# Kernel tuning notes

Measured on AMD Instinct MI355X. Metric: run time of the kernel, lower is better.

Reference implementation:

```python
import jax, jax.numpy as jnp
import numpy as np

E = 256      # embed_dim
H = 4        # num_heads
EXP = 4      # expansion_factor
B, C, R = 8, 32, 255  # batch, max_cols, rows (seq = R+1 with CLS)
LN_EPS = 1e-5


def setup_inputs() -> dict:
    key = jax.random.key(0)
    ks = jax.random.split(key, 16)
    s = 0.02
    return {
        "x": jax.random.normal(ks[0], (B, C, R, E), jnp.float32),
        "real_cols": jax.random.randint(ks[1], (B,), 0, C + 1),
        "real_rows": jax.random.randint(ks[2], (B,), 0, R + 1),
        "cls_token": jax.random.normal(ks[3], (E,), jnp.float32) * s,
        # MHA in_proj (torch packs q,k,v as (3E, E)) and out_proj
        "w_qkv": jax.random.normal(ks[4], (3 * E, E), jnp.float32) * s,
        "b_qkv": jnp.zeros((3 * E,), jnp.float32),
        "w_out": jax.random.normal(ks[5], (E, E), jnp.float32) * s,
        "b_out": jnp.zeros((E,), jnp.float32),
        # LayerNorm
        "ln_g": jnp.ones((E,), jnp.float32),
        "ln_b": jnp.zeros((E,), jnp.float32),
        # FFN: Linear(E, 4E) -> ReLU -> Linear(4E, E)
        "w1": jax.random.normal(ks[6], (EXP * E, E), jnp.float32) * s,
        "b1": jnp.zeros((EXP * E,), jnp.float32),
        "w2": jax.random.normal(ks[7], (E, EXP * E), jnp.float32) * s,
        "b2": jnp.zeros((E,), jnp.float32),
    }


def reference(x, real_cols, real_rows, cls_token, w_qkv, b_qkv, w_out, b_out,
              ln_g, ln_b, w1, b1, w2, b2):
    Bn, Cn, Rn, En = x.shape
    S = Rn + 1
    Dh = En // H
    dt = x.dtype

    # prepend CLS token to every column's row sequence -> (B, C, S, E)
    cls = jnp.broadcast_to(cls_token.astype(dt), (Bn, Cn, 1, En))
    xc = jnp.concatenate([cls, x], axis=2)

    # fused qkv projection
    qkv = jnp.einsum('bcse,fe->bcsf', xc, w_qkv.astype(dt)) + b_qkv.astype(dt)
    q, k, v = jnp.split(qkv, 3, axis=-1)
    q = q.reshape(Bn, Cn, S, H, Dh)
    k = k.reshape(Bn, Cn, S, H, Dh)
    v = v.reshape(Bn, Cn, S, H, Dh)

    scale = 1.0 / np.sqrt(Dh).astype(np.float32)
    scores = jnp.einsum('bcqhd,bckhd->bchqk', q, k) * scale  # (B,C,H,S,S)

    # key_padding_mask: position 0 (CLS) always valid; row p (1..R) valid iff p <= nrow
    pos = jnp.arange(S)
    valid = (pos[None, :] == 0) | (pos[None, :] <= real_rows[:, None])  # (B, S)
    neg = jnp.asarray(-1e9, scores.dtype)
    scores = jnp.where(valid[:, None, None, None, :], scores, neg)

    attn = jax.nn.softmax(scores, axis=-1)
    ctx = jnp.einsum('bchqk,bckhd->bcqhd', attn, v).reshape(Bn, Cn, S, En)
    mha = jnp.einsum('bcse,fe->bcsf', ctx, w_out.astype(dt)) + b_out.astype(dt)

    # LayerNorm over E
    mu = mha.mean(axis=-1, keepdims=True)
    var = ((mha - mu) ** 2).mean(axis=-1, keepdims=True)
    ln = (mha - mu) * jax.lax.rsqrt(var + LN_EPS) * ln_g.astype(dt) + ln_b.astype(dt)

    # FFN with residual from ln (out = ln + ffn(ln))
    h = jax.nn.relu(jnp.einsum('bcse,fe->bcsf', ln, w1.astype(dt)) + b1.astype(dt))
    ffn = jnp.einsum('bcsf,ef->bcse', h, w2.astype(dt)) + b2.astype(dt)
    out = ln + ffn

    # rep_mode == 'cls': take CLS position; zero out padded columns
    rep = out[:, :, 0, :]  # (B, C, E)
    col_valid = (jnp.arange(Cn)[None, :] < real_cols[:, None]).astype(dt)
    return rep * col_valid[..., None]
```

## Files before the change

kernel.cpp:

```cpp
#include <hip/hip_runtime.h>
#include <hip/hip_bf16.h>
#include <math.h>

static constexpr int kC = 32, kR = 255, kE = 256;

__device__ float g_q0kv[768];
__device__ float g_qw[4 * 256];
__device__ float g_s0[4];
__device__ float g_qb[4];
__device__ float g_m[256 * 4 * 4];
__device__ float g_l[256 * 4 * 4];
__device__ float g_part[256 * 4 * 4 * 256];
__device__ unsigned short g_wv_bf[256 * 256];
__device__ unsigned short g_wout_bf[256 * 256];
__device__ unsigned short g_w1_bf[1024 * 256];
__device__ unsigned short g_w2_bf[256 * 1024];

__device__ inline unsigned short f2bf(float f) {
  __hip_bfloat16 h = __float2bfloat16(f);
  return __builtin_bit_cast(unsigned short, h);
}
__device__ inline float bflo(unsigned int u) { return __uint_as_float(u << 16); }
__device__ inline float bfhi(unsigned int u) { return __uint_as_float(u & 0xffff0000u); }

__global__ __launch_bounds__(256) void k_heads(const float* __restrict__ cls,
                                               const float* __restrict__ w_qkv,
                                               const float* __restrict__ b_qkv) {
  const int t = threadIdx.x, wvi = t >> 6, l = t & 63;
  const int h = blockIdx.x;
  __shared__ float q0h[64];
  __shared__ float kch[64];
  {
    const int r = t >> 1, half = t & 1;
    const int row = (r < 64) ? (h * 64 + r) : (256 + h * 64 + (r - 64));
    const float4* wp = (const float4*)(w_qkv + (size_t)row * 256 + half * 128);
    const float4* cp = (const float4*)cls + half * 32;
    float a = 0.f;
#pragma unroll 8
    for (int j = 0; j < 32; ++j) {
      float4 w4 = wp[j];
      float4 cv = cp[j];
      a += w4.x * cv.x + w4.y * cv.y + w4.z * cv.z + w4.w * cv.w;
    }
    a += __shfl_xor(a, 1);
    if (half == 0) {
      const float val = a + b_qkv[row];
      if (r < 64) q0h[r] = val; else kch[r - 64] = val;
    }
  }
  __syncthreads();

  float acc = 0.f;
#pragma unroll 8
  for (int j = 0; j < 64; ++j)
    acc += q0h[j] * w_qkv[(size_t)(256 + h * 64 + j) * 256 + t];
  g_qw[h * 256 + t] = acc * 0.125f;
  if (wvi == 0) {
    const float q = q0h[l];
    float pk = q * kch[l];
    float pb = q * b_qkv[256 + h * 64 + l];
#pragma unroll
    for (int m = 1; m < 64; m <<= 1) {
      pk += __shfl_xor(pk, m);
      pb += __shfl_xor(pb, m);
    }
    if (l == 0) {
      g_s0[h] = pk * 0.125f;
      g_qb[h] = pb * 0.125f;
    }
  }
}

__global__ __launch_bounds__(256) void k_attn(const float* __restrict__ x,
                                              const int* __restrict__ real_cols,
                                              const int* __restrict__ real_rows,
                                              const float* __restrict__ cls,
                                              const float* __restrict__ w_qkv,
                                              const float* __restrict__ b_qkv,
                                              const float* __restrict__ w_out,
                                              const float* __restrict__ w1,
                                              const float* __restrict__ w2) {
  const int t = threadIdx.x, wv = t >> 6, l = t & 63;
  const int bid = blockIdx.x;
  __shared__ __align__(16) char smem[71680];

  if (bid >= 1064) {
    const int row = 512 + (bid - 1064) * 4 + wv;
    float4 w4 = *((const float4*)(w_qkv + (size_t)row * 256) + l);
    float4 c4 = *((const float4*)cls + l);
    float a = w4.x * c4.x + w4.y * c4.y + w4.z * c4.z + w4.w * c4.w;
#pragma unroll
    for (int m = 1; m < 64; m <<= 1) a += __shfl_xor(a, m);
    if (l == 0) g_q0kv[row] = a + b_qkv[row];
    return;
  }

  if (bid >= 1024) {
    const int u = bid - 1024;
    const float* src;
    unsigned short* dst;
    int R, C, o0, e0;
    if (u < 4) { src = w_qkv + 512 * 256; dst = g_wv_bf; R = 256; C = 256; o0 = u * 64; e0 = 0; }
    else if (u < 8) { src = w_out; dst = g_wout_bf; R = 256; C = 256; o0 = (u - 4) * 64; e0 = 0; }
    else if (u < 24) { src = w1; dst = g_w1_bf; R = 1024; C = 256; o0 = (u - 8) * 64; e0 = 0; }
    else { const int v = u - 24; src = w2; dst = g_w2_bf; R = 256; C = 1024; o0 = (v >> 2) * 64; e0 = (v & 3) * 256; }

    unsigned short* tile = (unsigned short*)smem;
    for (int r = wv; r < 64; r += 4) {
      float4 v = *((const float4*)(src + (size_t)(o0 + r) * C + e0) + l);
      ushort4 ov;
      ov.x = f2bf(v.x); ov.y = f2bf(v.y); ov.z = f2bf(v.z); ov.w = f2bf(v.w);
      *(ushort4*)&tile[r * 260 + 4 * l] = ov;
    }
    __syncthreads();
    const int e80 = e0 >> 3;
    for (int e8l = wv; e8l < 32; e8l += 4) {
      const unsigned int* tp = (const unsigned int*)&tile[l * 260 + e8l * 8];
      uint4 o;
      o.x = tp[0]; o.y = tp[1]; o.z = tp[2]; o.w = tp[3];
      *(uint4*)(dst + ((size_t)(e80 + e8l) * R + o0 + l) * 8) = o;
    }
    return;
  }

  const int bc = bid >> 2, chunk = bid & 3;
  const int b = bc >> 5, c = bc & 31;
  if (c >= real_cols[b]) return;
  const int rr = real_rows[b];
  const int r0 = chunk * 64;
  const int nr = min(64, rr - r0);
  if (nr <= 0) return;

  float (*xs)[260] = (float(*)[260])smem;
  float (*qws)[256] = (float(*)[256])(smem + 66560);
  float (*ps)[64] = (float(*)[64])(smem + 70656);

#pragma unroll
  for (int i = 0; i < 4; ++i) qws[i][t] = g_qw[i * 256 + t];

  const float* xb = x + ((size_t)bc * kR + r0) * kE;
  for (int r = wv; r < nr; r += 4)
    *(float4*)&xs[r][4 * l] = *(const float4*)(xb + (size_t)r * kE + 4 * l);
  __syncthreads();

  const int h = wv, row = l;
  float acc = 0.f;
  const float4* qrow = (const float4*)&qws[h][0];
  const float4* xrow = (const float4*)&xs[row][0];
#pragma unroll 8
  for (int e4 = 0; e4 < 64; ++e4) {
    float4 q4 = qrow[e4];
    float4 x4 = xrow[e4];
    acc += q4.x * x4.x + q4.y * x4.y + q4.z * x4.z + q4.w * x4.w;
  }
  float s = (row < nr) ? acc + g_qb[h] : -1e30f;
  float mx = s;
#pragma unroll
  for (int m = 1; m < 64; m <<= 1) mx = fmaxf(mx, __shfl_xor(mx, m));
  float p = (row < nr) ? __expf(s - mx) : 0.f;
  float lsum = p;
#pragma unroll
  for (int m = 1; m < 64; m <<= 1) lsum += __shfl_xor(lsum, m);
  ps[h][row] = p;
  if (l == 0) {
    g_m[(bc * 4 + chunk) * 4 + h] = mx;
    g_l[(bc * 4 + chunk) * 4 + h] = lsum;
  }
  __syncthreads();

  float a0 = 0.f, a1 = 0.f, a2 = 0.f, a3 = 0.f;
  for (int r2 = 0; r2 < nr; ++r2) {
    float xv = xs[r2][t];
    a0 += ps[0][r2] * xv;
    a1 += ps[1][r2] * xv;
    a2 += ps[2][r2] * xv;
    a3 += ps[3][r2] * xv;
  }
  float* pp = g_part + (size_t)(bc * 4 + chunk) * 4 * 256;
  pp[0 * 256 + t] = a0;
  pp[1 * 256 + t] = a1;
  pp[2 * 256 + t] = a2;
  pp[3 * 256 + t] = a3;
}

__global__ __launch_bounds__(1024) void k_token(const int* __restrict__ real_cols,
                                                const int* __restrict__ real_rows,
                                                const float* __restrict__ b_qkv,
                                                const float* __restrict__ b_out,
                                                const float* __restrict__ ln_g,
                                                const float* __restrict__ ln_b,
                                                const float* __restrict__ b1,
                                                const float* __restrict__ b2,
                                                float* __restrict__ out) {
  const int bc = blockIdx.x, b = bc >> 5, c = bc & 31;
  const int t = threadIdx.x, wv = t >> 6, l = t & 63;
  if (c >= real_cols[b]) {
    if (t < 256) out[(size_t)bc * 256 + t] = 0.f;
    return;
  }
  const int rr = real_rows[b];
  const int nch = (rr + 63) >> 6;

  __shared__ float xb[4][256];
  __shared__ float part[4][256];
  __shared__ float ctxs[256];
  __shared__ float lns[256];
  __shared__ float hs[1024];
  __shared__ float al[4][4];
  __shared__ float p0s[4];
  __shared__ float rb[2][4];

  if (t < 4) {
    const int h = t;
    const float s0 = g_s0[h];
    float M = s0;
    for (int ch = 0; ch < nch; ++ch) M = fmaxf(M, g_m[(bc * 4 + ch) * 4 + h]);
    float lt = __expf(s0 - M);
    const float w0 = lt;
    float av[4] = {0.f, 0.f, 0.f, 0.f};
    for (int ch = 0; ch < nch; ++ch) {
      float e = __expf(g_m[(bc * 4 + ch) * 4 + h] - M);
      av[ch] = e;
      lt += g_l[(bc * 4 + ch) * 4 + h] * e;
    }
    const float inv = 1.f / lt;
#pragma unroll
    for (int ch = 0; ch < 4; ++ch) al[h][ch] = av[ch] * inv;
    p0s[h] = w0 * inv;
  }
  __syncthreads();

  {
    const int h = t >> 8, e = t & 255;
    float a = 0.f;
    for (int ch = 0; ch < nch; ++ch)
      a += al[h][ch] * g_part[(size_t)(bc * 4 + ch) * 4 * 256 + h * 256 + e];
    xb[h][e] = a;
  }
  __syncthreads();

  {
    const int f = t & 255, q = t >> 8, h = f >> 6;
    const uint4* wr = (const uint4*)g_wv_bf;
    const float4* v4p = (const float4*)&xb[h][0];
    float acc = 0.f;
#pragma unroll
    for (int i = 0; i < 8; ++i) {
      const int e8 = q * 8 + i;
      uint4 w = wr[e8 * 256 + f];
      float4 a = v4p[2 * e8], bb = v4p[2 * e8 + 1];
      acc += bflo(w.x) * a.x + bfhi(w.x) * a.y + bflo(w.y) * a.z + bfhi(w.y) * a.w +
             bflo(w.z) * bb.x + bfhi(w.z) * bb.y + bflo(w.w) * bb.z + bfhi(w.w) * bb.w;
    }
    part[q][f] = acc;
  }
  __syncthreads();
  if (t < 256) {
    const int h = t >> 6;
    const float p0 = p0s[h];
    ctxs[t] = part[0][t] + part[1][t] + part[2][t] + part[3][t] +
              p0 * g_q0kv[512 + t] + (1.f - p0) * b_qkv[512 + t];
  }
  __syncthreads();

  {
    const int g = t & 255, q = t >> 8;
    const uint4* wr = (const uint4*)g_wout_bf;
    const float4* c4 = (const float4*)&ctxs[0];
    float acc = 0.f;
#pragma unroll
    for (int i = 0; i < 8; ++i) {
      const int e8 = q * 8 + i;
      uint4 w = wr[e8 * 256 + g];
      float4 a = c4[2 * e8], bb = c4[2 * e8 + 1];
      acc += bflo(w.x) * a.x + bfhi(w.x) * a.y + bflo(w.y) * a.z + bfhi(w.y) * a.w +
             bflo(w.z) * bb.x + bfhi(w.z) * bb.y + bflo(w.w) * bb.z + bfhi(w.w) * bb.w;
    }
    part[q][g] = acc;
  }
  __syncthreads();
  float mh = 0.f;
  if (t < 256) {
    mh = part[0][t] + part[1][t] + part[2][t] + part[3][t] + b_out[t];
    float s1 = mh, s2 = mh * mh;
#pragma unroll
    for (int m = 1; m < 64; m <<= 1) {
      s1 += __shfl_xor(s1, m);
      s2 += __shfl_xor(s2, m);
    }
    if (l == 0) {
      rb[0][wv] = s1;
      rb[1][wv] = s2;
    }
  }
  __syncthreads();
  if (t < 256) {
    const float mu = (rb[0][0] + rb[0][1] + rb[0][2] + rb[0][3]) * (1.f / 256.f);
    const float msq = (rb[1][0] + rb[1][1] + rb[1][2] + rb[1][3]) * (1.f / 256.f);
    const float var = msq - mu * mu;
    lns[t] = (mh - mu) * rsqrtf(var + 1e-5f) * ln_g[t] + ln_b[t];
  }
  __syncthreads();

  {
    const uint4* wr = (const uint4*)g_w1_bf;
    float acc = b1[t];
#pragma unroll
    for (int e8 = 0; e8 < 32; ++e8) {
      uint4 w = wr[e8 * 1024 + t];
      const float4 a = *(const float4*)&lns[8 * e8];
      const float4 bbv = *(const float4*)&lns[8 * e8 + 4];
      acc += bflo(w.x) * a.x + bfhi(w.x) * a.y + bflo(w.y) * a.z + bfhi(w.y) * a.w +
             bflo(w.z) * bbv.x + bfhi(w.z) * bbv.y + bflo(w.w) * bbv.z + bfhi(w.w) * bbv.w;
    }
    hs[t] = fmaxf(acc, 0.f);
  }
  __syncthreads();

  {
    const int e = t & 255, q = t >> 8;
    const uint4* wr = (const uint4*)g_w2_bf;
    const float4* h4 = (const float4*)&hs[0];
    float acc = 0.f;
#pragma unroll 8
    for (int i = 0; i < 32; ++i) {
      const int f8 = q * 32 + i;
      uint4 w = wr[f8 * 256 + e];
      float4 a = h4[2 * f8], bb = h4[2 * f8 + 1];
      acc += bflo(w.x) * a.x + bfhi(w.x) * a.y + bflo(w.y) * a.z + bfhi(w.y) * a.w +
             bflo(w.z) * bb.x + bfhi(w.z) * bb.y + bflo(w.w) * bb.z + bfhi(w.w) * bb.w;
    }
    part[q][e] = acc;
  }
  __syncthreads();
  if (t < 256)
    out[(size_t)bc * 256 + t] =
        lns[t] + part[0][t] + part[1][t] + part[2][t] + part[3][t] + b2[t];
}

extern "C" void kernel_launch(void* const* d_in, const int* in_sizes, int n_in,
                              void* d_out, int out_size, void* d_ws, size_t ws_size,
                              hipStream_t stream) {
  const float* x = (const float*)d_in[0];
  const int* real_cols = (const int*)d_in[1];
  const int* real_rows = (const int*)d_in[2];
  const float* cls = (const float*)d_in[3];
  const float* w_qkv = (const float*)d_in[4];
  const float* b_qkv = (const float*)d_in[5];
  const float* w_out = (const float*)d_in[6];
  const float* b_out = (const float*)d_in[7];
  const float* ln_g = (const float*)d_in[8];
  const float* ln_b = (const float*)d_in[9];
  const float* w1 = (const float*)d_in[10];
  const float* b1 = (const float*)d_in[11];
  const float* w2 = (const float*)d_in[12];
  const float* b2 = (const float*)d_in[13];
  float* out = (float*)d_out;
  (void)in_sizes; (void)n_in; (void)out_size; (void)d_ws; (void)ws_size;

  k_heads<<<4, 256, 0, stream>>>(cls, w_qkv, b_qkv);
  k_attn<<<1128, 256, 0, stream>>>(x, real_cols, real_rows, cls, w_qkv, b_qkv, w_out, w1, w2);
  k_token<<<256, 1024, 0, stream>>>(real_cols, real_rows, b_qkv, b_out, ln_g, ln_b, b1, b2, out);
}
```

Before: 154.7 us.

## Split attention into 32-row chunks and move FFN into token-batched kernels

Attention row chunks shrink from 64 to 32 rows, doubling the number of k_attn blocks and halving shared memory per block to raise occupancy and parallelism. The per-token tail kernel now stops after LayerNorm and writes the normalized vector to global memory. The FFN runs in two new grid-parallel kernels that each process four tokens per block, so every bf16 weight load is reused across tokens and the work spreads across more blocks. The cost is two extra launches plus global round-trips for the LN output and the hidden activations, and in the 32-row chunks half of each wave's lanes do redundant dot products.

```diff
diff --git a/kernel.cpp b/kernel.cpp
--- a/kernel.cpp
+++ b/kernel.cpp
@@ -8,9 +8,11 @@
 __device__ float g_qw[4 * 256];
 __device__ float g_s0[4];
 __device__ float g_qb[4];
-__device__ float g_m[256 * 4 * 4];
-__device__ float g_l[256 * 4 * 4];
-__device__ float g_part[256 * 4 * 4 * 256];
+__device__ float g_m[256 * 8 * 4];
+__device__ float g_l[256 * 8 * 4];
+__device__ float g_part[256 * 8 * 4 * 256];
+__device__ float g_ln[256 * 256];
+__device__ float g_hact[256 * 1024];
 __device__ unsigned short g_wv_bf[256 * 256];
 __device__ unsigned short g_wout_bf[256 * 256];
 __device__ unsigned short g_w1_bf[1024 * 256];
@@ -82,10 +84,10 @@
                                               const float* __restrict__ w2) {
   const int t = threadIdx.x, wv = t >> 6, l = t & 63;
   const int bid = blockIdx.x;
-  __shared__ __align__(16) char smem[71680];
-
-  if (bid >= 1064) {
-    const int row = 512 + (bid - 1064) * 4 + wv;
+  __shared__ __align__(16) char smem[37888];
+
+  if (bid >= 2088) {
+    const int row = 512 + (bid - 2088) * 4 + wv;
     float4 w4 = *((const float4*)(w_qkv + (size_t)row * 256) + l);
     float4 c4 = *((const float4*)cls + l);
     float a = w4.x * c4.x + w4.y * c4.y + w4.z * c4.z + w4.w * c4.w;
@@ -95,8 +97,8 @@
     return;
   }
 
-  if (bid >= 1024) {
-    const int u = bid - 1024;
+  if (bid >= 2048) {
+    const int u = bid - 2048;
     const float* src;
     unsigned short* dst;
     int R, C, o0, e0;
@@ -123,17 +125,17 @@
     return;
   }
 
-  const int bc = bid >> 2, chunk = bid & 3;
+  const int bc = bid >> 3, chunk = bid & 7;
   const int b = bc >> 5, c = bc & 31;
   if (c >= real_cols[b]) return;
   const int rr = real_rows[b];
-  const int r0 = chunk * 64;
-  const int nr = min(64, rr - r0);
+  const int r0 = chunk * 32;
+  const int nr = min(32, rr - r0);
   if (nr <= 0) return;
 
   float (*xs)[260] = (float(*)[260])smem;
-  float (*qws)[256] = (float(*)[256])(smem + 66560);
-  float (*ps)[64] = (float(*)[64])(smem + 70656);
+  float (*qws)[256] = (float(*)[256])(smem + 33280);
+  float (*ps)[32] = (float(*)[32])(smem + 37376);
 
 #pragma unroll
   for (int i = 0; i < 4; ++i) qws[i][t] = g_qw[i * 256 + t];
@@ -146,7 +148,7 @@
   const int h = wv, row = l;
   float acc = 0.f;
   const float4* qrow = (const float4*)&qws[h][0];
-  const float4* xrow = (const float4*)&xs[row][0];
+  const float4* xrow = (const float4*)&xs[row < 32 ? row : 0][0];
 #pragma unroll 8
   for (int e4 = 0; e4 < 64; ++e4) {
     float4 q4 = qrow[e4];
@@ -161,10 +163,10 @@
   float lsum = p;
 #pragma unroll
   for (int m = 1; m < 64; m <<= 1) lsum += __shfl_xor(lsum, m);
-  ps[h][row] = p;
+  if (row < 32) ps[h][row] = p;
   if (l == 0) {
-    g_m[(bc * 4 + chunk) * 4 + h] = mx;
-    g_l[(bc * 4 + chunk) * 4 + h] = lsum;
+    g_m[(bc * 8 + chunk) * 4 + h] = mx;
+    g_l[(bc * 8 + chunk) * 4 + h] = lsum;
   }
   __syncthreads();
 
@@ -176,37 +178,29 @@
     a2 += ps[2][r2] * xv;
     a3 += ps[3][r2] * xv;
   }
-  float* pp = g_part + (size_t)(bc * 4 + chunk) * 4 * 256;
+  float* pp = g_part + (size_t)(bc * 8 + chunk) * 4 * 256;
   pp[0 * 256 + t] = a0;
   pp[1 * 256 + t] = a1;
   pp[2 * 256 + t] = a2;
   pp[3 * 256 + t] = a3;
 }
 
-__global__ __launch_bounds__(1024) void k_token(const int* __restrict__ real_cols,
-                                                const int* __restrict__ real_rows,
-                                                const float* __restrict__ b_qkv,
-                                                const float* __restrict__ b_out,
-                                                const float* __restrict__ ln_g,
-                                                const float* __restrict__ ln_b,
-                                                const float* __restrict__ b1,
-                                                const float* __restrict__ b2,
-                                                float* __restrict__ out) {
+__global__ __launch_bounds__(1024) void k_tail(const int* __restrict__ real_cols,
+                                               const int* __restrict__ real_rows,
+                                               const float* __restrict__ b_qkv,
+                                               const float* __restrict__ b_out,
+                                               const float* __restrict__ ln_g,
+                                               const float* __restrict__ ln_b) {
   const int bc = blockIdx.x, b = bc >> 5, c = bc & 31;
   const int t = threadIdx.x, wv = t >> 6, l = t & 63;
-  if (c >= real_cols[b]) {
-    if (t < 256) out[(size_t)bc * 256 + t] = 0.f;
-    return;
-  }
+  if (c >= real_cols[b]) return;
   const int rr = real_rows[b];
-  const int nch = (rr + 63) >> 6;
+  const int nch = (rr + 31) >> 5;
 
   __shared__ float xb[4][256];
   __shared__ float part[4][256];
   __shared__ float ctxs[256];
-  __shared__ float lns[256];
-  __shared__ float hs[1024];
-  __shared__ float al[4][4];
+  __shared__ float al[4][8];
   __shared__ float p0s[4];
   __shared__ float rb[2][4];
 
@@ -214,18 +208,18 @@
     const int h = t;
     const float s0 = g_s0[h];
     float M = s0;
-    for (int ch = 0; ch < nch; ++ch) M = fmaxf(M, g_m[(bc * 4 + ch) * 4 + h]);
+    for (int ch = 0; ch < nch; ++ch) M = fmaxf(M, g_m[(bc * 8 + ch) * 4 + h]);
     float lt = __expf(s0 - M);
     const float w0 = lt;
-    float av[4] = {0.f, 0.f, 0.f, 0.f};
+    float av[8] = {0.f, 0.f, 0.f, 0.f, 0.f, 0.f, 0.f, 0.f};
     for (int ch = 0; ch < nch; ++ch) {
-      float e = __expf(g_m[(bc * 4 + ch) * 4 + h] - M);
+      float e = __expf(g_m[(bc * 8 + ch) * 4 + h] - M);
       av[ch] = e;
-      lt += g_l[(bc * 4 + ch) * 4 + h] * e;
+      lt += g_l[(bc * 8 + ch) * 4 + h] * e;
     }
     const float inv = 1.f / lt;
 #pragma unroll
-    for (int ch = 0; ch < 4; ++ch) al[h][ch] = av[ch] * inv;
+    for (int ch = 0; ch < 8; ++ch) al[h][ch] = av[ch] * inv;
     p0s[h] = w0 * inv;
   }
   __syncthreads();
@@ -234,7 +228,7 @@
     const int h = t >> 8, e = t & 255;
     float a = 0.f;
     for (int ch = 0; ch < nch; ++ch)
-      a += al[h][ch] * g_part[(size_t)(bc * 4 + ch) * 4 * 256 + h * 256 + e];
+      a += al[h][ch] * g_part[(size_t)(bc * 8 + ch) * 4 * 256 + h * 256 + e];
     xb[h][e] = a;
   }
   __syncthreads();
@@ -279,9 +273,8 @@
     part[q][g] = acc;
   }
   __syncthreads();
-  float mh = 0.f;
   if (t < 256) {
-    mh = part[0][t] + part[1][t] + part[2][t] + part[3][t] + b_out[t];
+    const float mh = part[0][t] + part[1][t] + part[2][t] + part[3][t] + b_out[t];
     float s1 = mh, s2 = mh * mh;
 #pragma unroll
     for (int m = 1; m < 64; m <<= 1) {
@@ -292,50 +285,91 @@
       rb[0][wv] = s1;
       rb[1][wv] = s2;
     }
-  }
-  __syncthreads();
-  if (t < 256) {
+    __syncthreads();
     const float mu = (rb[0][0] + rb[0][1] + rb[0][2] + rb[0][3]) * (1.f / 256.f);
     const float msq = (rb[1][0] + rb[1][1] + rb[1][2] + rb[1][3]) * (1.f / 256.f);
     const float var = msq - mu * mu;
-    lns[t] = (mh - mu) * rsqrtf(var + 1e-5f) * ln_g[t] + ln_b[t];
-  }
-  __syncthreads();
-
+    g_ln[(size_t)bc * 256 + t] =
+        (mh - mu) * rsqrtf(var + 1e-5f) * ln_g[t] + ln_b[t];
+  } else {
+    __syncthreads();
+  }
+}
+
+__global__ __launch_bounds__(256) void k_ffn1(const float* __restrict__ b1,
+                                              const int* __restrict__ real_cols) {
+  const int tok0 = blockIdx.x * 4;
+  const int b = tok0 >> 5, c0 = tok0 & 31;
+  if (c0 >= real_cols[b]) return;
+  __shared__ float lns[4][256];
+  const int t = threadIdx.x;
+  const int f0 = blockIdx.y * 128;
+#pragma unroll
+  for (int i = 0; i < 4; ++i) lns[i][t] = g_ln[(size_t)(tok0 + i) * 256 + t];
+  __syncthreads();
+  const int f = f0 + (t & 127), tp = t >> 7;
+  const uint4* wr = (const uint4*)g_w1_bf;
+  const float bb = b1[f];
+  float acc0 = bb, acc1 = bb;
+  const float4* l0 = (const float4*)&lns[tp * 2][0];
+  const float4* l1 = (const float4*)&lns[tp * 2 + 1][0];
+#pragma unroll 8
+  for (int e8 = 0; e8 < 32; ++e8) {
+    uint4 w = wr[e8 * 1024 + f];
+    const float w0 = bflo(w.x), w1v = bfhi(w.x), w2v = bflo(w.y), w3 = bfhi(w.y);
+    const float w4v = bflo(w.z), w5 = bfhi(w.z), w6 = bflo(w.w), w7 = bfhi(w.w);
+    float4 a = l0[2 * e8], bbv = l0[2 * e8 + 1];
+    acc0 += w0 * a.x + w1v * a.y + w2v * a.z + w3 * a.w +
+            w4v * bbv.x + w5 * bbv.y + w6 * bbv.z + w7 * bbv.w;
+    a = l1[2 * e8]; bbv = l1[2 * e8 + 1];
+    acc1 += w0 * a.x + w1v * a.y + w2v * a.z + w3 * a.w +
+            w4v * bbv.x + w5 * bbv.y + w6 * bbv.z + w7 * bbv.w;
+  }
+  g_hact[(size_t)(tok0 + tp * 2) * 1024 + f] = fmaxf(acc0, 0.f);
+  g_hact[(size_t)(tok0 + tp * 2 + 1) * 1024 + f] = fmaxf(acc1, 0.f);
+}
+
+__global__ __launch_bounds__(256) void k_ffn2(const float* __restrict__ b2,
+                                              const int* __restrict__ real_cols,
+                                              float* __restrict__ out) {
+  const int t = threadIdx.x;
+  const int tok0 = blockIdx.x * 4, e0 = blockIdx.y * 32;
+  const int b = tok0 >> 5, c0 = tok0 & 31;
+  const int ncols = real_cols[b];
+  if (c0 >= ncols) {
+    if (t < 128) out[(size_t)(tok0 + (t >> 5)) * 256 + e0 + (t & 31)] = 0.f;
+    return;
+  }
+  __shared__ float hs[4][1024];
+  __shared__ float part[2][4][32];
   {
-    const uint4* wr = (const uint4*)g_w1_bf;
-    float acc = b1[t];
-#pragma unroll
-    for (int e8 = 0; e8 < 32; ++e8) {
-      uint4 w = wr[e8 * 1024 + t];
-      const float4 a = *(const float4*)&lns[8 * e8];
-      const float4 bbv = *(const float4*)&lns[8 * e8 + 4];
-      acc += bflo(w.x) * a.x + bfhi(w.x) * a.y + bflo(w.y) * a.z + bfhi(w.y) * a.w +
-             bflo(w.z) * bbv.x + bfhi(w.z) * bbv.y + bflo(w.w) * bbv.z + bfhi(w.w) * bbv.w;
-    }
-    hs[t] = fmaxf(acc, 0.f);
-  }
-  __syncthreads();
-
-  {
-    const int e = t & 255, q = t >> 8;
-    const uint4* wr = (const uint4*)g_w2_bf;
-    const float4* h4 = (const float4*)&hs[0];
-    float acc = 0.f;
+    const float4* hsrc = (const float4*)(g_hact + (size_t)tok0 * 1024);
+    float4* hd = (float4*)&hs[0][0];
+#pragma unroll
+    for (int j = 0; j < 4; ++j) hd[t + 256 * j] = hsrc[t + 256 * j];
+  }
+  __syncthreads();
+  const int e = e0 + (t & 31), i = (t >> 5) & 3, q = t >> 7;
+  const uint4* wr = (const uint4*)g_w2_bf;
+  const float4* h4 = (const float4*)&hs[i][0];
+  float acc = 0.f;
 #pragma unroll 8
-    for (int i = 0; i < 32; ++i) {
-      const int f8 = q * 32 + i;
-      uint4 w = wr[f8 * 256 + e];
-      float4 a = h4[2 * f8], bb = h4[2 * f8 + 1];
-      acc += bflo(w.x) * a.x + bfhi(w.x) * a.y + bflo(w.y) * a.z + bfhi(w.y) * a.w +
-             bflo(w.z) * bb.x + bfhi(w.z) * bb.y + bflo(w.w) * bb.z + bfhi(w.w) * bb.w;
-    }
-    part[q][e] = acc;
-  }
-  __syncthreads();
-  if (t < 256)
-    out[(size_t)bc * 256 + t] =
-        lns[t] + part[0][t] + part[1][t] + part[2][t] + part[3][t] + b2[t];
+  for (int f8i = 0; f8i < 64; ++f8i) {
+    const int f8 = q * 64 + f8i;
+    uint4 w = wr[f8 * 256 + e];
+    float4 a = h4[2 * f8], bb = h4[2 * f8 + 1];
+    acc += bflo(w.x) * a.x + bfhi(w.x) * a.y + bflo(w.y) * a.z + bfhi(w.y) * a.w +
+           bflo(w.z) * bb.x + bfhi(w.z) * bb.y + bflo(w.w) * bb.z + bfhi(w.w) * bb.w;
+  }
+  part[q][i][t & 31] = acc;
+  __syncthreads();
+  if (t < 128) {
+    const int ii = t >> 5, ee = e0 + (t & 31);
+    const int tok = tok0 + ii, c = tok & 31;
+    const float r = part[0][ii][t & 31] + part[1][ii][t & 31] + b2[ee];
+    const float lnv = g_ln[(size_t)tok * 256 + ee];
+    out[(size_t)tok * 256 + ee] = (c < ncols) ? (lnv + r) : 0.f;
+  }
 }
 
 extern "C" void kernel_launch(void* const* d_in, const int* in_sizes, int n_in,
@@ -359,6 +393,8 @@
   (void)in_sizes; (void)n_in; (void)out_size; (void)d_ws; (void)ws_size;
 
   k_heads<<<4, 256, 0, stream>>>(cls, w_qkv, b_qkv);
-  k_attn<<<1128, 256, 0, stream>>>(x, real_cols, real_rows, cls, w_qkv, b_qkv, w_out, w1, w2);
-  k_token<<<256, 1024, 0, stream>>>(real_cols, real_rows, b_qkv, b_out, ln_g, ln_b, b1, b2, out);
-}
+  k_attn<<<2152, 256, 0, stream>>>(x, real_cols, real_rows, cls, w_qkv, b_qkv, w_out, w1, w2);
+  k_tail<<<256, 1024, 0, stream>>>(real_cols, real_rows, b_qkv, b_out, ln_g, ln_b);
+  k_ffn1<<<dim3(64, 8), 256, 0, stream>>>(b1, real_cols);
+  k_ffn2<<<dim3(64, 8), 256, 0, stream>>>(b2, real_cols, out);
+}
```

Result: slower. 181.4 us (+17.2%).

## Process two tokens per block in k_token to reuse bf16 weight loads

Applied to the files above, without the earlier changes.

Each k_token block now handles two (batch, column) tokens, j and j+128, and the grid shrinks from 256 to 128 blocks. Every bf16 weight vector loaded in the V, out-projection, FFN1 and FFN2 matvecs is applied to both tokens, halving weight traffic per token. Padded columns are still zeroed, but the block runs the full compute if either of its two tokens is valid, so some dead work appears. Fewer blocks means less parallelism across CUs, and shared memory and register use roughly double.

```diff
diff --git a/kernel.cpp b/kernel.cpp
--- a/kernel.cpp
+++ b/kernel.cpp
@@ -192,26 +192,36 @@
                                                 const float* __restrict__ b1,
                                                 const float* __restrict__ b2,
                                                 float* __restrict__ out) {
-  const int bc = blockIdx.x, b = bc >> 5, c = bc & 31;
+  const int j = blockIdx.x;
+  const int bc0 = j, bc1 = j + 128;
+  const int b0 = bc0 >> 5, c0 = bc0 & 31;
+  const int b1i = bc1 >> 5, c1 = bc1 & 31;
   const int t = threadIdx.x, wv = t >> 6, l = t & 63;
-  if (c >= real_cols[b]) {
-    if (t < 256) out[(size_t)bc * 256 + t] = 0.f;
+  const bool valid0 = (c0 < real_cols[b0]);
+  const bool valid1 = (c1 < real_cols[b1i]);
+  if (!valid0 && !valid1) {
+    if (t < 256) {
+      out[(size_t)bc0 * 256 + t] = 0.f;
+      out[(size_t)bc1 * 256 + t] = 0.f;
+    }
     return;
   }
-  const int rr = real_rows[b];
-  const int nch = (rr + 63) >> 6;
-
-  __shared__ float xb[4][256];
-  __shared__ float part[4][256];
-  __shared__ float ctxs[256];
-  __shared__ float lns[256];
-  __shared__ float hs[1024];
-  __shared__ float al[4][4];
-  __shared__ float p0s[4];
-  __shared__ float rb[2][4];
-
-  if (t < 4) {
-    const int h = t;
+  const int nch0 = (real_rows[b0] + 63) >> 6;
+  const int nch1 = (real_rows[b1i] + 63) >> 6;
+
+  __shared__ float xb[2][4][256];
+  __shared__ float part[4][2][256];
+  __shared__ float ctxs[2][256];
+  __shared__ float lns[2][256];
+  __shared__ float hs[2][1024];
+  __shared__ float al[2][4][4];
+  __shared__ float p0s[2][4];
+  __shared__ float rb[2][2][4];
+
+  if (t < 8) {
+    const int sel = t >> 2, h = t & 3;
+    const int bc = sel ? bc1 : bc0;
+    const int nch = sel ? nch1 : nch0;
     const float s0 = g_s0[h];
     float M = s0;
     for (int ch = 0; ch < nch; ++ch) M = fmaxf(M, g_m[(bc * 4 + ch) * 4 + h]);
@@ -225,117 +235,156 @@
     }
     const float inv = 1.f / lt;
 #pragma unroll
-    for (int ch = 0; ch < 4; ++ch) al[h][ch] = av[ch] * inv;
-    p0s[h] = w0 * inv;
+    for (int ch = 0; ch < 4; ++ch) al[sel][h][ch] = av[ch] * inv;
+    p0s[sel][h] = w0 * inv;
   }
   __syncthreads();
 
   {
     const int h = t >> 8, e = t & 255;
-    float a = 0.f;
-    for (int ch = 0; ch < nch; ++ch)
-      a += al[h][ch] * g_part[(size_t)(bc * 4 + ch) * 4 * 256 + h * 256 + e];
-    xb[h][e] = a;
+    float a0 = 0.f, a1 = 0.f;
+    for (int ch = 0; ch < nch0; ++ch)
+      a0 += al[0][h][ch] * g_part[(size_t)(bc0 * 4 + ch) * 4 * 256 + h * 256 + e];
+    for (int ch = 0; ch < nch1; ++ch)
+      a1 += al[1][h][ch] * g_part[(size_t)(bc1 * 4 + ch) * 4 * 256 + h * 256 + e];
+    xb[0][h][e] = a0;
+    xb[1][h][e] = a1;
   }
   __syncthreads();
 
   {
     const int f = t & 255, q = t >> 8, h = f >> 6;
     const uint4* wr = (const uint4*)g_wv_bf;
-    const float4* v4p = (const float4*)&xb[h][0];
-    float acc = 0.f;
+    const float4* v0 = (const float4*)&xb[0][h][0];
+    const float4* v1 = (const float4*)&xb[1][h][0];
+    float acc0 = 0.f, acc1 = 0.f;
 #pragma unroll
     for (int i = 0; i < 8; ++i) {
       const int e8 = q * 8 + i;
       uint4 w = wr[e8 * 256 + f];
-      float4 a = v4p[2 * e8], bb = v4p[2 * e8 + 1];
-      acc += bflo(w.x) * a.x + bfhi(w.x) * a.y + bflo(w.y) * a.z + bfhi(w.y) * a.w +
-             bflo(w.z) * bb.x + bfhi(w.z) * bb.y + bflo(w.w) * bb.z + bfhi(w.w) * bb.w;
-    }
-    part[q][f] = acc;
-  }
-  __syncthreads();
-  if (t < 256) {
-    const int h = t >> 6;
-    const float p0 = p0s[h];
-    ctxs[t] = part[0][t] + part[1][t] + part[2][t] + part[3][t] +
-              p0 * g_q0kv[512 + t] + (1.f - p0) * b_qkv[512 + t];
+      const float w0 = bflo(w.x), w1v = bfhi(w.x), w2v = bflo(w.y), w3 = bfhi(w.y);
+      const float w4v = bflo(w.z), w5 = bfhi(w.z), w6 = bflo(w.w), w7 = bfhi(w.w);
+      float4 a = v0[2 * e8], bb = v0[2 * e8 + 1];
+      acc0 += w0 * a.x + w1v * a.y + w2v * a.z + w3 * a.w +
+              w4v * bb.x + w5 * bb.y + w6 * bb.z + w7 * bb.w;
+      a = v1[2 * e8]; bb = v1[2 * e8 + 1];
+      acc1 += w0 * a.x + w1v * a.y + w2v * a.z + w3 * a.w +
+              w4v * bb.x + w5 * bb.y + w6 * bb.z + w7 * bb.w;
+    }
+    part[q][0][f] = acc0;
+    part[q][1][f] = acc1;
+  }
+  __syncthreads();
+  if (t < 512) {
+    const int sel = t >> 8, f = t & 255, h = f >> 6;
+    const float p0 = p0s[sel][h];
+    ctxs[sel][f] = part[0][sel][f] + part[1][sel][f] + part[2][sel][f] + part[3][sel][f] +
+                   p0 * g_q0kv[512 + f] + (1.f - p0) * b_qkv[512 + f];
   }
   __syncthreads();
 
   {
     const int g = t & 255, q = t >> 8;
     const uint4* wr = (const uint4*)g_wout_bf;
-    const float4* c4 = (const float4*)&ctxs[0];
-    float acc = 0.f;
+    const float4* c0p = (const float4*)&ctxs[0][0];
+    const float4* c1p = (const float4*)&ctxs[1][0];
+    float acc0 = 0.f, acc1 = 0.f;
 #pragma unroll
     for (int i = 0; i < 8; ++i) {
       const int e8 = q * 8 + i;
       uint4 w = wr[e8 * 256 + g];
-      float4 a = c4[2 * e8], bb = c4[2 * e8 + 1];
-      acc += bflo(w.x) * a.x + bfhi(w.x) * a.y + bflo(w.y) * a.z + bfhi(w.y) * a.w +
-             bflo(w.z) * bb.x + bfhi(w.z) * bb.y + bflo(w.w) * bb.z + bfhi(w.w) * bb.w;
-    }
-    part[q][g] = acc;
-  }
-  __syncthreads();
-  float mh = 0.f;
-  if (t < 256) {
-    mh = part[0][t] + part[1][t] + part[2][t] + part[3][t] + b_out[t];
+      const float w0 = bflo(w.x), w1v = bfhi(w.x), w2v = bflo(w.y), w3 = bfhi(w.y);
+      const float w4v = bflo(w.z), w5 = bfhi(w.z), w6 = bflo(w.w), w7 = bfhi(w.w);
+      float4 a = c0p[2 * e8], bb = c0p[2 * e8 + 1];
+      acc0 += w0 * a.x + w1v * a.y + w2v * a.z + w3 * a.w +
+              w4v * bb.x + w5 * bb.y + w6 * bb.z + w7 * bb.w;
+      a = c1p[2 * e8]; bb = c1p[2 * e8 + 1];
+      acc1 += w0 * a.x + w1v * a.y + w2v * a.z + w3 * a.w +
+              w4v * bb.x + w5 * bb.y + w6 * bb.z + w7 * bb.w;
+    }
+    part[q][0][g] = acc0;
+    part[q][1][g] = acc1;
+  }
+  __syncthreads();
+
+  {
+    float mh = 0.f;
+    const int sel = t >> 8, g = t & 255;
+    if (t < 512)
+      mh = part[0][sel][g] + part[1][sel][g] + part[2][sel][g] + part[3][sel][g] + b_out[g];
     float s1 = mh, s2 = mh * mh;
 #pragma unroll
     for (int m = 1; m < 64; m <<= 1) {
       s1 += __shfl_xor(s1, m);
       s2 += __shfl_xor(s2, m);
     }
-    if (l == 0) {
-      rb[0][wv] = s1;
-      rb[1][wv] = s2;
-    }
-  }
-  __syncthreads();
-  if (t < 256) {
-    const float mu = (rb[0][0] + rb[0][1] + rb[0][2] + rb[0][3]) * (1.f / 256.f);
-    const float msq = (rb[1][0] + rb[1][1] + rb[1][2] + rb[1][3]) * (1.f / 256.f);
-    const float var = msq - mu * mu;
-    lns[t] = (mh - mu) * rsqrtf(var + 1e-5f) * ln_g[t] + ln_b[t];
-  }
-  __syncthreads();
+    if (t < 512 && l == 0) {
+      rb[0][sel][wv & 3] = s1;
+      rb[1][sel][wv & 3] = s2;
+    }
+    __syncthreads();
+    if (t < 512) {
+      const float mu = (rb[0][sel][0] + rb[0][sel][1] + rb[0][sel][2] + rb[0][sel][3]) * (1.f / 256.f);
+      const float msq = (rb[1][sel][0] + rb[1][sel][1] + rb[1][sel][2] + rb[1][sel][3]) * (1.f / 256.f);
+      const float var = msq - mu * mu;
+      lns[sel][g] = (mh - mu) * rsqrtf(var + 1e-5f) * ln_g[g] + ln_b[g];
+    }
+    __syncthreads();
+  }
 
   {
     const uint4* wr = (const uint4*)g_w1_bf;
-    float acc = b1[t];
-#pragma unroll
+    const float bb1 = b1[t];
+    float acc0 = bb1, acc1 = bb1;
+    const float4* l0 = (const float4*)&lns[0][0];
+    const float4* l1 = (const float4*)&lns[1][0];
+#pragma unroll 8
     for (int e8 = 0; e8 < 32; ++e8) {
       uint4 w = wr[e8 * 1024 + t];
-      const float4 a = *(const float4*)&lns[8 * e8];
-      const float4 bbv = *(const float4*)&lns[8 * e8 + 4];
-      acc += bflo(w.x) * a.x + bfhi(w.x) * a.y + bflo(w.y) * a.z + bfhi(w.y) * a.w +
-             bflo(w.z) * bbv.x + bfhi(w.z) * bbv.y + bflo(w.w) * bbv.z + bfhi(w.w) * bbv.w;
-    }
-    hs[t] = fmaxf(acc, 0.f);
+      const float w0 = bflo(w.x), w1v = bfhi(w.x), w2v = bflo(w.y), w3 = bfhi(w.y);
+      const float w4v = bflo(w.z), w5 = bfhi(w.z), w6 = bflo(w.w), w7 = bfhi(w.w);
+      float4 a = l0[2 * e8], bbv = l0[2 * e8 + 1];
+      acc0 += w0 * a.x + w1v * a.y + w2v * a.z + w3 * a.w +
+              w4v * bbv.x + w5 * bbv.y + w6 * bbv.z + w7 * bbv.w;
+      a = l1[2 * e8]; bbv = l1[2 * e8 + 1];
+      acc1 += w0 * a.x + w1v * a.y + w2v * a.z + w3 * a.w +
+              w4v * bbv.x + w5 * bbv.y + w6 * bbv.z + w7 * bbv.w;
+    }
+    hs[0][t] = fmaxf(acc0, 0.f);
+    hs[1][t] = fmaxf(acc1, 0.f);
   }
   __syncthreads();
 
   {
     const int e = t & 255, q = t >> 8;
     const uint4* wr = (const uint4*)g_w2_bf;
-    const float4* h4 = (const float4*)&hs[0];
-    float acc = 0.f;
+    const float4* h0 = (const float4*)&hs[0][0];
+    const float4* h1 = (const float4*)&hs[1][0];
+    float acc0 = 0.f, acc1 = 0.f;
 #pragma unroll 8
     for (int i = 0; i < 32; ++i) {
       const int f8 = q * 32 + i;
       uint4 w = wr[f8 * 256 + e];
-      float4 a = h4[2 * f8], bb = h4[2 * f8 + 1];
-      acc += bflo(w.x) * a.x + bfhi(w.x) * a.y + bflo(w.y) * a.z + bfhi(w.y) * a.w +
-             bflo(w.z) * bb.x + bfhi(w.z) * bb.y + bflo(w.w) * bb.z + bfhi(w.w) * bb.w;
-    }
-    part[q][e] = acc;
-  }
-  __syncthreads();
-  if (t < 256)
-    out[(size_t)bc * 256 + t] =
-        lns[t] + part[0][t] + part[1][t] + part[2][t] + part[3][t] + b2[t];
+      const float w0 = bflo(w.x), w1v = bfhi(w.x), w2v = bflo(w.y), w3 = bfhi(w.y);
+      const float w4v = bflo(w.z), w5 = bfhi(w.z), w6 = bflo(w.w), w7 = bfhi(w.w);
+      float4 a = h0[2 * f8], bb = h0[2 * f8 + 1];
+      acc0 += w0 * a.x + w1v * a.y + w2v * a.z + w3 * a.w +
+              w4v * bb.x + w5 * bb.y + w6 * bb.z + w7 * bb.w;
+      a = h1[2 * f8]; bb = h1[2 * f8 + 1];
+      acc1 += w0 * a.x + w1v * a.y + w2v * a.z + w3 * a.w +
+              w4v * bb.x + w5 * bb.y + w6 * bb.z + w7 * bb.w;
+    }
+    part[q][0][e] = acc0;
+    part[q][1][e] = acc1;
+  }
+  __syncthreads();
+  if (t < 512) {
+    const int sel = t >> 8, e = t & 255;
+    const int bc = sel ? bc1 : bc0;
+    const bool valid = sel ? valid1 : valid0;
+    const float r = part[0][sel][e] + part[1][sel][e] + part[2][sel][e] + part[3][sel][e] + b2[e];
+    out[(size_t)bc * 256 + e] = valid ? (lns[sel][e] + r) : 0.f;
+  }
 }
 
 extern "C" void kernel_launch(void* const* d_in, const int* in_sizes, int n_in,
@@ -360,5 +409,5 @@
 
   k_heads<<<4, 256, 0, stream>>>(cls, w_qkv, b_qkv);
   k_attn<<<1128, 256, 0, stream>>>(x, real_cols, real_rows, cls, w_qkv, b_qkv, w_out, w1, w2);
-  k_token<<<256, 1024, 0, stream>>>(real_cols, real_rows, b_qkv, b_out, ln_g, ln_b, b1, b2, out);
+  k_token<<<128, 1024, 0, stream>>>(real_cols, real_rows, b_qkv, b_out, ln_g, ln_b, b1, b2, out);
 }
```

New measurement: 166.1 us. +7.3%, slower.

## Batch 16 tokens per block and run tail projections with bf16 MFMA

Applied to the files above, without the earlier changes.

The per-token GEMV tail kernel (256 blocks) becomes a batched kernel where each of 16 blocks handles 16 column tokens. The V-projection, out-projection and FFN matmuls now run on 16x16x32 bf16 MFMA instructions, so each weight load is shared across 16 tokens. The V and out-projection inputs are split into hi/lo bf16 pairs to keep precision. Weight conversion now writes plain row-major bf16 instead of a transposed layout, and intermediates go through global scratch buffers. The cost is far fewer blocks in flight, extra global round-trips, and full computation for any block that holds at least one valid column.

```diff
diff --git a/kernel.cpp b/kernel.cpp
--- a/kernel.cpp
+++ b/kernel.cpp
@@ -3,6 +3,9 @@
 #include <math.h>
 
 static constexpr int kC = 32, kR = 255, kE = 256;
+
+typedef float f32x4 __attribute__((ext_vector_type(4)));
+typedef short bf16x8 __attribute__((ext_vector_type(8)));
 
 __device__ float g_q0kv[768];
 __device__ float g_qw[4 * 256];
@@ -11,17 +14,26 @@
 __device__ float g_m[256 * 4 * 4];
 __device__ float g_l[256 * 4 * 4];
 __device__ float g_part[256 * 4 * 4 * 256];
-__device__ unsigned short g_wv_bf[256 * 256];
-__device__ unsigned short g_wout_bf[256 * 256];
-__device__ unsigned short g_w1_bf[1024 * 256];
-__device__ unsigned short g_w2_bf[256 * 1024];
+
+__device__ unsigned short g_wv_rm[256 * 256];
+__device__ unsigned short g_wout_rm[256 * 256];
+__device__ unsigned short g_w1_rm[1024 * 256];
+__device__ unsigned short g_w2_rm[256 * 1024];
+
+#define XH_S 1056
+#define CT_S 264
+__device__ unsigned short g_xh[256 * XH_S], g_xl[256 * XH_S];
+__device__ unsigned short g_ctxh[256 * CT_S], g_ctxl[256 * CT_S];
+__device__ unsigned short g_lnsb[256 * CT_S];
+__device__ unsigned short g_hsb[256 * XH_S];
 
 __device__ inline unsigned short f2bf(float f) {
   __hip_bfloat16 h = __float2bfloat16(f);
   return __builtin_bit_cast(unsigned short, h);
 }
-__device__ inline float bflo(unsigned int u) { return __uint_as_float(u << 16); }
-__device__ inline float bfhi(unsigned int u) { return __uint_as_float(u & 0xffff0000u); }
+__device__ inline float bf2f(unsigned short u) {
+  return __uint_as_float(((unsigned)u) << 16);
+}
 
 __global__ __launch_bounds__(256) void k_heads(const float* __restrict__ cls,
                                                const float* __restrict__ w_qkv,
@@ -99,26 +111,18 @@
     const int u = bid - 1024;
     const float* src;
     unsigned short* dst;
-    int R, C, o0, e0;
-    if (u < 4) { src = w_qkv + 512 * 256; dst = g_wv_bf; R = 256; C = 256; o0 = u * 64; e0 = 0; }
-    else if (u < 8) { src = w_out; dst = g_wout_bf; R = 256; C = 256; o0 = (u - 4) * 64; e0 = 0; }
-    else if (u < 24) { src = w1; dst = g_w1_bf; R = 1024; C = 256; o0 = (u - 8) * 64; e0 = 0; }
-    else { const int v = u - 24; src = w2; dst = g_w2_bf; R = 256; C = 1024; o0 = (v >> 2) * 64; e0 = (v & 3) * 256; }
-
-    unsigned short* tile = (unsigned short*)smem;
-    for (int r = wv; r < 64; r += 4) {
-      float4 v = *((const float4*)(src + (size_t)(o0 + r) * C + e0) + l);
-      ushort4 ov;
-      ov.x = f2bf(v.x); ov.y = f2bf(v.y); ov.z = f2bf(v.z); ov.w = f2bf(v.w);
-      *(ushort4*)&tile[r * 260 + 4 * l] = ov;
-    }
-    __syncthreads();
-    const int e80 = e0 >> 3;
-    for (int e8l = wv; e8l < 32; e8l += 4) {
-      const unsigned int* tp = (const unsigned int*)&tile[l * 260 + e8l * 8];
-      uint4 o;
-      o.x = tp[0]; o.y = tp[1]; o.z = tp[2]; o.w = tp[3];
-      *(uint4*)(dst + ((size_t)(e80 + e8l) * R + o0 + l) * 8) = o;
+    if (u < 4) { src = w_qkv + 512 * 256 + u * 16384; dst = g_wv_rm + u * 16384; }
+    else if (u < 8) { src = w_out + (u - 4) * 16384; dst = g_wout_rm + (u - 4) * 16384; }
+    else if (u < 24) { src = w1 + (u - 8) * 16384; dst = g_w1_rm + (u - 8) * 16384; }
+    else { src = w2 + (u - 24) * 16384; dst = g_w2_rm + (u - 24) * 16384; }
+    const float4* s4 = (const float4*)src;
+    ushort4* d4 = (ushort4*)dst;
+#pragma unroll 4
+    for (int i = 0; i < 16; ++i) {
+      float4 v = s4[i * 256 + t];
+      ushort4 o;
+      o.x = f2bf(v.x); o.y = f2bf(v.y); o.z = f2bf(v.z); o.w = f2bf(v.w);
+      d4[i * 256 + t] = o;
     }
     return;
   }
@@ -183,35 +187,35 @@
   pp[3 * 256 + t] = a3;
 }
 
-__global__ __launch_bounds__(1024) void k_token(const int* __restrict__ real_cols,
-                                                const int* __restrict__ real_rows,
-                                                const float* __restrict__ b_qkv,
-                                                const float* __restrict__ b_out,
-                                                const float* __restrict__ ln_g,
-                                                const float* __restrict__ ln_b,
-                                                const float* __restrict__ b1,
-                                                const float* __restrict__ b2,
-                                                float* __restrict__ out) {
-  const int bc = blockIdx.x, b = bc >> 5, c = bc & 31;
+__global__ __launch_bounds__(1024) void k_tail_mm(const int* __restrict__ real_cols,
+                                                  const int* __restrict__ real_rows,
+                                                  const float* __restrict__ b_qkv,
+                                                  const float* __restrict__ b_out,
+                                                  const float* __restrict__ ln_g,
+                                                  const float* __restrict__ ln_b,
+                                                  const float* __restrict__ b1,
+                                                  const float* __restrict__ b2,
+                                                  float* __restrict__ out) {
+  const int tg = blockIdx.x;
   const int t = threadIdx.x, wv = t >> 6, l = t & 63;
-  if (c >= real_cols[b]) {
-    if (t < 256) out[(size_t)bc * 256 + t] = 0.f;
+  const int bidx = tg >> 1;
+  const int ncols = real_cols[bidx];
+  if ((tg & 1) * 16 >= ncols) {
+    float4 z = {0.f, 0.f, 0.f, 0.f};
+    ((float4*)out)[(size_t)(tg * 16 + (t >> 6)) * 64 + (t & 63)] = z;
     return;
   }
-  const int rr = real_rows[b];
-  const int nch = (rr + 63) >> 6;
-
-  __shared__ float xb[4][256];
-  __shared__ float part[4][256];
-  __shared__ float ctxs[256];
-  __shared__ float lns[256];
-  __shared__ float hs[1024];
-  __shared__ float al[4][4];
-  __shared__ float p0s[4];
-  __shared__ float rb[2][4];
-
-  if (t < 4) {
-    const int h = t;
+  const int nch = (real_rows[bidx] + 63) >> 6;
+
+  __shared__ float s_mh[16 * 257];
+  __shared__ float s_lnf[16 * 260];
+  __shared__ float s_al[16][4][4];
+  __shared__ float s_p0[16][4];
+  __shared__ float s_redS[16], s_redQ[16];
+
+  if (t < 64) {
+    const int tok = t >> 2, h = t & 3;
+    const int bc = tg * 16 + tok;
     const float s0 = g_s0[h];
     float M = s0;
     for (int ch = 0; ch < nch; ++ch) M = fmaxf(M, g_m[(bc * 4 + ch) * 4 + h]);
@@ -225,117 +229,155 @@
     }
     const float inv = 1.f / lt;
 #pragma unroll
-    for (int ch = 0; ch < 4; ++ch) al[h][ch] = av[ch] * inv;
-    p0s[h] = w0 * inv;
-  }
-  __syncthreads();
-
-  {
-    const int h = t >> 8, e = t & 255;
-    float a = 0.f;
-    for (int ch = 0; ch < nch; ++ch)
-      a += al[h][ch] * g_part[(size_t)(bc * 4 + ch) * 4 * 256 + h * 256 + e];
-    xb[h][e] = a;
-  }
-  __syncthreads();
-
-  {
-    const int f = t & 255, q = t >> 8, h = f >> 6;
-    const uint4* wr = (const uint4*)g_wv_bf;
-    const float4* v4p = (const float4*)&xb[h][0];
-    float acc = 0.f;
-#pragma unroll
-    for (int i = 0; i < 8; ++i) {
-      const int e8 = q * 8 + i;
-      uint4 w = wr[e8 * 256 + f];
-      float4 a = v4p[2 * e8], bb = v4p[2 * e8 + 1];
-      acc += bflo(w.x) * a.x + bfhi(w.x) * a.y + bflo(w.y) * a.z + bfhi(w.y) * a.w +
-             bflo(w.z) * bb.x + bfhi(w.z) * bb.y + bflo(w.w) * bb.z + bfhi(w.w) * bb.w;
-    }
-    part[q][f] = acc;
-  }
-  __syncthreads();
+    for (int ch = 0; ch < 4; ++ch) s_al[tok][h][ch] = av[ch] * inv;
+    s_p0[tok][h] = w0 * inv;
+  }
+  __syncthreads();
+
+  {
+    const int tok = t >> 6, j = t & 63;
+    const int bc = tg * 16 + tok;
+#pragma unroll
+    for (int h = 0; h < 4; ++h) {
+      float4 a = {0.f, 0.f, 0.f, 0.f};
+      for (int ch = 0; ch < nch; ++ch) {
+        const float al = s_al[tok][h][ch];
+        const float4 p = *(const float4*)(g_part + (size_t)(bc * 4 + ch) * 1024 + h * 256 + j * 4);
+        a.x += al * p.x; a.y += al * p.y; a.z += al * p.z; a.w += al * p.w;
+      }
+      ushort4 hi, lo;
+      hi.x = f2bf(a.x); lo.x = f2bf(a.x - bf2f(hi.x));
+      hi.y = f2bf(a.y); lo.y = f2bf(a.y - bf2f(hi.y));
+      hi.z = f2bf(a.z); lo.z = f2bf(a.z - bf2f(hi.z));
+      hi.w = f2bf(a.w); lo.w = f2bf(a.w - bf2f(hi.w));
+      *(ushort4*)(g_xh + (size_t)bc * XH_S + h * 256 + j * 4) = hi;
+      *(ushort4*)(g_xl + (size_t)bc * XH_S + h * 256 + j * 4) = lo;
+    }
+  }
+  __syncthreads();
+
+  const int r = l & 15, q = l >> 4;
+  const int bcr = tg * 16 + r;
+
+  {
+    const int h = wv >> 2, f0 = h * 64 + (wv & 3) * 16;
+    const unsigned short* wa = g_wv_rm + (size_t)(f0 + r) * 256 + 8 * q;
+    const unsigned short* xh = g_xh + (size_t)bcr * XH_S + h * 256 + 8 * q;
+    const unsigned short* xl = g_xl + (size_t)bcr * XH_S + h * 256 + 8 * q;
+    f32x4 acc = {0.f, 0.f, 0.f, 0.f};
+#pragma unroll
+    for (int ks = 0; ks < 8; ++ks) {
+      bf16x8 a = *(const bf16x8*)(wa + ks * 32);
+      acc = __builtin_amdgcn_mfma_f32_16x16x32_bf16(a, *(const bf16x8*)(xh + ks * 32), acc, 0, 0, 0);
+      acc = __builtin_amdgcn_mfma_f32_16x16x32_bf16(a, *(const bf16x8*)(xl + ks * 32), acc, 0, 0, 0);
+    }
+    const float p0 = s_p0[r][h];
+#pragma unroll
+    for (int i = 0; i < 4; ++i) {
+      const int f = f0 + q * 4 + i;
+      const float v = acc[i] + p0 * g_q0kv[512 + f] + (1.f - p0) * b_qkv[512 + f];
+      const unsigned short hu = f2bf(v);
+      g_ctxh[(size_t)bcr * CT_S + f] = hu;
+      g_ctxl[(size_t)bcr * CT_S + f] = f2bf(v - bf2f(hu));
+    }
+  }
+  __syncthreads();
+
+  {
+    const int g0 = wv * 16;
+    const unsigned short* wa = g_wout_rm + (size_t)(g0 + r) * 256 + 8 * q;
+    const unsigned short* ch_ = g_ctxh + (size_t)bcr * CT_S + 8 * q;
+    const unsigned short* cl_ = g_ctxl + (size_t)bcr * CT_S + 8 * q;
+    f32x4 acc = {0.f, 0.f, 0.f, 0.f};
+#pragma unroll
+    for (int ks = 0; ks < 8; ++ks) {
+      bf16x8 a = *(const bf16x8*)(wa + ks * 32);
+      acc = __builtin_amdgcn_mfma_f32_16x16x32_bf16(a, *(const bf16x8*)(ch_ + ks * 32), acc, 0, 0, 0);
+      acc = __builtin_amdgcn_mfma_f32_16x16x32_bf16(a, *(const bf16x8*)(cl_ + ks * 32), acc, 0, 0, 0);
+    }
+#pragma unroll
+    for (int i = 0; i < 4; ++i) {
+      const int g = g0 + q * 4 + i;
+      s_mh[r * 257 + g] = acc[i] + b_out[g];
+    }
+  }
+  __syncthreads();
+
   if (t < 256) {
-    const int h = t >> 6;
-    const float p0 = p0s[h];
-    ctxs[t] = part[0][t] + part[1][t] + part[2][t] + part[3][t] +
-              p0 * g_q0kv[512 + t] + (1.f - p0) * b_qkv[512 + t];
-  }
-  __syncthreads();
-
-  {
-    const int g = t & 255, q = t >> 8;
-    const uint4* wr = (const uint4*)g_wout_bf;
-    const float4* c4 = (const float4*)&ctxs[0];
-    float acc = 0.f;
-#pragma unroll
-    for (int i = 0; i < 8; ++i) {
-      const int e8 = q * 8 + i;
-      uint4 w = wr[e8 * 256 + g];
-      float4 a = c4[2 * e8], bb = c4[2 * e8 + 1];
-      acc += bflo(w.x) * a.x + bfhi(w.x) * a.y + bflo(w.y) * a.z + bfhi(w.y) * a.w +
-             bflo(w.z) * bb.x + bfhi(w.z) * bb.y + bflo(w.w) * bb.z + bfhi(w.w) * bb.w;
-    }
-    part[q][g] = acc;
-  }
-  __syncthreads();
-  float mh = 0.f;
-  if (t < 256) {
-    mh = part[0][t] + part[1][t] + part[2][t] + part[3][t] + b_out[t];
-    float s1 = mh, s2 = mh * mh;
-#pragma unroll
-    for (int m = 1; m < 64; m <<= 1) {
+    const int tok = t >> 4, seg = t & 15;
+    float s1 = 0.f, s2 = 0.f;
+#pragma unroll
+    for (int i = 0; i < 16; ++i) {
+      const float v = s_mh[tok * 257 + seg * 16 + i];
+      s1 += v; s2 += v * v;
+    }
+#pragma unroll
+    for (int m = 1; m < 16; m <<= 1) {
       s1 += __shfl_xor(s1, m);
       s2 += __shfl_xor(s2, m);
     }
-    if (l == 0) {
-      rb[0][wv] = s1;
-      rb[1][wv] = s2;
-    }
-  }
-  __syncthreads();
-  if (t < 256) {
-    const float mu = (rb[0][0] + rb[0][1] + rb[0][2] + rb[0][3]) * (1.f / 256.f);
-    const float msq = (rb[1][0] + rb[1][1] + rb[1][2] + rb[1][3]) * (1.f / 256.f);
-    const float var = msq - mu * mu;
-    lns[t] = (mh - mu) * rsqrtf(var + 1e-5f) * ln_g[t] + ln_b[t];
-  }
-  __syncthreads();
-
-  {
-    const uint4* wr = (const uint4*)g_w1_bf;
-    float acc = b1[t];
-#pragma unroll
-    for (int e8 = 0; e8 < 32; ++e8) {
-      uint4 w = wr[e8 * 1024 + t];
-      const float4 a = *(const float4*)&lns[8 * e8];
-      const float4 bbv = *(const float4*)&lns[8 * e8 + 4];
-      acc += bflo(w.x) * a.x + bfhi(w.x) * a.y + bflo(w.y) * a.z + bfhi(w.y) * a.w +
-             bflo(w.z) * bbv.x + bfhi(w.z) * bbv.y + bflo(w.w) * bbv.z + bfhi(w.w) * bbv.w;
-    }
-    hs[t] = fmaxf(acc, 0.f);
-  }
-  __syncthreads();
-
-  {
-    const int e = t & 255, q = t >> 8;
-    const uint4* wr = (const uint4*)g_w2_bf;
-    const float4* h4 = (const float4*)&hs[0];
-    float acc = 0.f;
+    if (seg == 0) { s_redS[tok] = s1; s_redQ[tok] = s2; }
+  }
+  __syncthreads();
+
+  {
+    const int tok = t >> 6, e4 = t & 63;
+    const float mu = s_redS[tok] * (1.f / 256.f);
+    const float var = s_redQ[tok] * (1.f / 256.f) - mu * mu;
+    const float rs = rsqrtf(var + 1e-5f);
+    const float4 gg = *((const float4*)ln_g + e4);
+    const float4 bb = *((const float4*)ln_b + e4);
+    float4 o;
+    o.x = (s_mh[tok * 257 + e4 * 4 + 0] - mu) * rs * gg.x + bb.x;
+    o.y = (s_mh[tok * 257 + e4 * 4 + 1] - mu) * rs * gg.y + bb.y;
+    o.z = (s_mh[tok * 257 + e4 * 4 + 2] - mu) * rs * gg.z + bb.z;
+    o.w = (s_mh[tok * 257 + e4 * 4 + 3] - mu) * rs * gg.w + bb.w;
+    *(float4*)&s_lnf[tok * 260 + e4 * 4] = o;
+    ushort4 ob;
+    ob.x = f2bf(o.x); ob.y = f2bf(o.y); ob.z = f2bf(o.z); ob.w = f2bf(o.w);
+    *(ushort4*)(g_lnsb + (size_t)(tg * 16 + tok) * CT_S + e4 * 4) = ob;
+  }
+  __syncthreads();
+
+  {
+    const unsigned short* lb = g_lnsb + (size_t)bcr * CT_S + 8 * q;
+#pragma unroll
+    for (int mt = 0; mt < 4; ++mt) {
+      const int f0 = wv * 64 + mt * 16;
+      const unsigned short* wa = g_w1_rm + (size_t)(f0 + r) * 256 + 8 * q;
+      f32x4 acc = {0.f, 0.f, 0.f, 0.f};
+#pragma unroll
+      for (int ks = 0; ks < 8; ++ks) {
+        acc = __builtin_amdgcn_mfma_f32_16x16x32_bf16(
+            *(const bf16x8*)(wa + ks * 32), *(const bf16x8*)(lb + ks * 32), acc, 0, 0, 0);
+      }
+#pragma unroll
+      for (int i = 0; i < 4; ++i) {
+        const int f = f0 + q * 4 + i;
+        g_hsb[(size_t)bcr * XH_S + f] = f2bf(fmaxf(acc[i] + b1[f], 0.f));
+      }
+    }
+  }
+  __syncthreads();
+
+  {
+    const int e0 = wv * 16;
+    const unsigned short* wa = g_w2_rm + (size_t)(e0 + r) * 1024 + 8 * q;
+    const unsigned short* hb = g_hsb + (size_t)bcr * XH_S + 8 * q;
+    f32x4 acc = {0.f, 0.f, 0.f, 0.f};
 #pragma unroll 8
-    for (int i = 0; i < 32; ++i) {
-      const int f8 = q * 32 + i;
-      uint4 w = wr[f8 * 256 + e];
-      float4 a = h4[2 * f8], bb = h4[2 * f8 + 1];
-      acc += bflo(w.x) * a.x + bfhi(w.x) * a.y + bflo(w.y) * a.z + bfhi(w.y) * a.w +
-             bflo(w.z) * bb.x + bfhi(w.z) * bb.y + bflo(w.w) * bb.z + bfhi(w.w) * bb.w;
-    }
-    part[q][e] = acc;
-  }
-  __syncthreads();
-  if (t < 256)
-    out[(size_t)bc * 256 + t] =
-        lns[t] + part[0][t] + part[1][t] + part[2][t] + part[3][t] + b2[t];
+    for (int ks = 0; ks < 32; ++ks) {
+      acc = __builtin_amdgcn_mfma_f32_16x16x32_bf16(
+          *(const bf16x8*)(wa + ks * 32), *(const bf16x8*)(hb + ks * 32), acc, 0, 0, 0);
+    }
+    const bool valid = ((tg & 1) * 16 + r) < ncols;
+#pragma unroll
+    for (int i = 0; i < 4; ++i) {
+      const int e = e0 + q * 4 + i;
+      const float v = s_lnf[r * 260 + e] + acc[i] + b2[e];
+      out[(size_t)bcr * 256 + e] = valid ? v : 0.f;
+    }
+  }
 }
 
 extern "C" void kernel_launch(void* const* d_in, const int* in_sizes, int n_in,
@@ -360,5 +402,5 @@
 
   k_heads<<<4, 256, 0, stream>>>(cls, w_qkv, b_qkv);
   k_attn<<<1128, 256, 0, stream>>>(x, real_cols, real_rows, cls, w_qkv, b_qkv, w_out, w1, w2);
-  k_token<<<256, 1024, 0, stream>>>(real_cols, real_rows, b_qkv, b_out, ln_g, ln_b, b1, b2, out);
-}
+  k_tail_mm<<<16, 1024, 0, stream>>>(real_cols, real_rows, b_qkv, b_out, ln_g, ln_b, b1, b2, out);
+}
```

Measured after the change: 205.9 us. +33.1%, slower.
